# Optimization experiments

Measured on AMD Instinct MI355X. Metric: run time of the kernel, lower is better.

Reference implementation:

```python
import jax, jax.numpy as jnp
import numpy as np

EMBED_DIM = 2048
NUM_HEADS = 32
NUM_KV_HEADS = 8
HEAD_DIM = EMBED_DIM // NUM_HEADS          # 64
GROUP = NUM_HEADS // NUM_KV_HEADS          # 4 queries per KV head
BATCH, SEQ = 2, 2048


def setup_inputs() -> dict:
    key = jax.random.key(0)
    ks = jax.random.split(key, 9)
    s_in = 1.0 / np.sqrt(EMBED_DIM)
    kv_dim = NUM_KV_HEADS * HEAD_DIM
    return {
        "x":      jax.random.normal(ks[0], (BATCH, SEQ, EMBED_DIM), jnp.float32),
        "Wq":     jax.random.normal(ks[1], (EMBED_DIM, EMBED_DIM), jnp.float32) * s_in,
        "bq":     jnp.zeros((EMBED_DIM,), jnp.float32),
        "Wk":     jax.random.normal(ks[2], (EMBED_DIM, kv_dim), jnp.float32) * s_in,
        "bk":     jnp.zeros((kv_dim,), jnp.float32),
        "Wv":     jax.random.normal(ks[3], (EMBED_DIM, kv_dim), jnp.float32) * s_in,
        "bv":     jnp.zeros((kv_dim,), jnp.float32),
        "Wo":     jax.random.normal(ks[4], (EMBED_DIM, EMBED_DIM), jnp.float32) * s_in,
        "bo":     jnp.zeros((EMBED_DIM,), jnp.float32),
    }


def reference(x, Wq, bq, Wk, bk, Wv, bv, Wo, bo):
    B, S, _ = x.shape
    # Projections (torch Linear == x @ W + b with W stored as [in, out] here)
    q = (x @ Wq + bq).reshape(B, S, NUM_KV_HEADS, GROUP, HEAD_DIM)  # grouped heads
    k = (x @ Wk + bk).reshape(B, S, NUM_KV_HEADS, HEAD_DIM)
    v = (x @ Wv + bv).reshape(B, S, NUM_KV_HEADS, HEAD_DIM)

    scale = 1.0 / np.sqrt(HEAD_DIM)
    # scores[b, h, g, s, t] = q[b, s, h, g, :] . k[b, t, h, :]
    # (repeat_interleave of K across the group dim == broadcasting over g)
    scores = jnp.einsum("bshgd,bthd->bhgst", q, k) * scale
    attn = jax.nn.softmax(scores, axis=-1)
    out = jnp.einsum("bhgst,bthd->bshgd", attn, v)  # [B, S, kvh, g, D]
    out = out.reshape(B, S, EMBED_DIM)
    return out @ Wo + bo
```

## Files before the change

### kernel.cpp

```cpp
#include <hip/hip_runtime.h>


typedef __attribute__((ext_vector_type(8)))  short     s16x8;
typedef __attribute__((ext_vector_type(8)))  _Float16  h8;
typedef __attribute__((ext_vector_type(2)))  __fp16    fp16x2;
typedef __attribute__((ext_vector_type(4)))  float     f32x4;
typedef __attribute__((ext_vector_type(16))) float     f32x16;

#define DEVI static __device__ __forceinline__

#if __has_builtin(__builtin_amdgcn_exp2f)
#define EXP2F __builtin_amdgcn_exp2f
#else
#define EXP2F exp2f
#endif

DEVI short f2h(float f){ _Float16 h = (_Float16)f; return __builtin_bit_cast(short, h); }
DEVI unsigned pkh(float a, float b){
  fp16x2 t = __builtin_amdgcn_cvt_pkrtz(a, b);
  return __builtin_bit_cast(unsigned, t);
}

typedef __attribute__((address_space(3))) unsigned       lds_u32;
typedef __attribute__((address_space(1))) const unsigned gbl_u32;
DEVI void glds16(const short* g, short* l){
  __builtin_amdgcn_global_load_lds((gbl_u32*)g, (lds_u32*)l, 16, 0, 0);
}

__global__ void cast_kernel(const float* __restrict__ in, short* __restrict__ out, int n){
  int i = (blockIdx.x * 256 + threadIdx.x) * 8;
  if(i >= n) return;
  float4 a = *(const float4*)(in + i);
  float4 b = *(const float4*)(in + i + 4);
  s16x8 v;
  v[0]=f2h(a.x); v[1]=f2h(a.y); v[2]=f2h(a.z); v[3]=f2h(a.w);
  v[4]=f2h(b.x); v[5]=f2h(b.y); v[6]=f2h(b.z); v[7]=f2h(b.w);
  *(s16x8*)(out + i) = v;
}

__global__ void prep_kernel(const float* __restrict__ Wq, const float* __restrict__ Wk,
                            const float* __restrict__ Wv, const float* __restrict__ Wo,
                            const float* __restrict__ bq, const float* __restrict__ bk,
                            const float* __restrict__ bv,
                            short* __restrict__ WT, short* __restrict__ WoT,
                            float* __restrict__ bqkv){
  __shared__ __align__(16) short tile[64*72];
  const int gy = blockIdx.y;
  const int t = threadIdx.x;
  if(gy >= 80){
    int i = blockIdx.x * 256 + t;
    if(i < 3072) bqkv[i] = (i < 2048) ? bq[i] : (i < 2560 ? bk[i-2048] : bv[i-2560]);
    return;
  }
  const float* src; short* dst; int ldin, by;
  if(gy < 32)      { src = Wq; dst = WT;             ldin = 2048; by = gy;    }
  else if(gy < 40) { src = Wk; dst = WT + 2048*2048; ldin =  512; by = gy-32; }
  else if(gy < 48) { src = Wv; dst = WT + 2560*2048; ldin =  512; by = gy-40; }
  else             { src = Wo; dst = WoT;            ldin = 2048; by = gy-48; }
  const int tr = blockIdx.x * 64;
  const int tc = by * 64;
  for(int c = t; c < 512; c += 256){
    int r = c >> 3, g = c & 7;
    const float* p = src + (size_t)(tr + r) * ldin + tc + g*8;
    s16x8 v;
    #pragma unroll
    for(int e = 0; e < 8; e++) v[e] = f2h(p[e]);
    *(s16x8*)&tile[r*72 + g*8] = v;
  }
  __syncthreads();
  for(int c = t; c < 512; c += 256){
    int r = c >> 3, g = c & 7;
    s16x8 v;
    #pragma unroll
    for(int e = 0; e < 8; e++) v[e] = tile[(g*8+e)*72 + r];
    *(s16x8*)(dst + (size_t)(tc + r) * 2048 + tr + g*8) = v;
  }
}

__global__ void transpose_h_kernel(const short* __restrict__ in, short* __restrict__ out,
                                   int ldin, int ldout){
  __shared__ __align__(16) short tile[64*72];
  const int tr = blockIdx.x * 64;
  const int tc = blockIdx.y * 64;
  const int t = threadIdx.x;
  for(int c = t; c < 512; c += 256){
    int r = c >> 3, g = c & 7;
    *(s16x8*)&tile[r*72 + g*8] = *(const s16x8*)(in + (size_t)(tr + r) * ldin + tc + g*8);
  }
  __syncthreads();
  for(int c = t; c < 512; c += 256){
    int r = c >> 3, g = c & 7;
    s16x8 v;
    #pragma unroll
    for(int e = 0; e < 8; e++) v[e] = tile[(g*8+e)*72 + r];
    *(s16x8*)(out + (size_t)(tc + r) * ldout + tr + g*8) = v;
  }
}

template<bool OUT_F32>
__global__ __launch_bounds__(256, 2)
void gemm_bt_kernel(const short* __restrict__ A, const short* __restrict__ BT,
                    const float* __restrict__ bias, void* __restrict__ C,
                    int M, int N, int K, int scale_cols, float qscale){
  __shared__ __align__(16) short As[128*32];
  __shared__ __align__(16) short Bs[128*32];
  const int m0 = blockIdx.x * 128;
  const int n0 = blockIdx.y * 128;
  const int tid = threadIdx.x;
  const int wave = tid >> 6, lane = tid & 63;
  const int l16 = lane & 15, quad = lane >> 4;
  const int wm = (wave >> 1) * 64, wn = (wave & 1) * 64;

  const short* gA = A  + (size_t)(m0 + wave*32 + (lane>>2))*K + (lane&3)*8;
  const short* gB = BT + (size_t)(n0 + wave*32 + (lane>>2))*K + (lane&3)*8;
  short* lA = As + wave*32*32;
  short* lB = Bs + wave*32*32;

  f32x4 acc[4][4];
  #pragma unroll
  for(int i=0;i<4;i++)
    #pragma unroll
    for(int j=0;j<4;j++) acc[i][j] = (f32x4)(0.0f);

  for(int k0 = 0; k0 < K; k0 += 32){
    glds16(gA + k0,                lA);
    glds16(gA + 16*(size_t)K + k0, lA + 512);
    glds16(gB + k0,                lB);
    glds16(gB + 16*(size_t)K + k0, lB + 512);
    __syncthreads();
    h8 af[4], bfr[4];
    #pragma unroll
    for(int i=0;i<4;i++){
      af[i]  = *(const h8*)&As[(wm + i*16 + l16)*32 + quad*8];
      bfr[i] = *(const h8*)&Bs[(wn + i*16 + l16)*32 + quad*8];
    }
    #pragma unroll
    for(int i=0;i<4;i++)
      #pragma unroll
      for(int j=0;j<4;j++)
        acc[i][j] = __builtin_amdgcn_mfma_f32_16x16x32_f16(af[i], bfr[j], acc[i][j], 0, 0, 0);
    __syncthreads();
  }

  #pragma unroll
  for(int j=0;j<4;j++){
    int col = n0 + wn + j*16 + l16;
    float bb = bias[col];
    float sc = (col < scale_cols) ? qscale : 1.0f;
    #pragma unroll
    for(int i=0;i<4;i++){
      #pragma unroll
      for(int r=0;r<4;r++){
        size_t row = (size_t)(m0 + wm + i*16 + quad*4 + r);
        float v = (acc[i][j][r] + bb) * sc;
        if(OUT_F32) ((float*)C)[row*(size_t)N + col] = v;
        else        ((short*)C)[row*(size_t)N + col] = f2h(v);
      }
    }
  }
}

__global__ __launch_bounds__(256, 2)
void attn_kernel(const short* __restrict__ Qg, const short* __restrict__ Kg,
                 const short* __restrict__ VT, short* __restrict__ Og, int ldq){
  const int qt  = blockIdx.x;
  const int kvh = blockIdx.y;
  const int b   = blockIdx.z;
  const int tid = threadIdx.x;
  const int wave = tid >> 6, lane = tid & 63;
  const int c = lane & 31, h = lane >> 5;
  const int head = kvh*4 + wave;
  const int q0 = qt * 64;

  __shared__ __align__(16) short Ks[2][64*72];
  __shared__ __align__(16) short Vs[2][64*72];

  h8 qreg[4][2];
  #pragma unroll
  for(int ks2=0; ks2<4; ks2++)
    #pragma unroll
    for(int qg=0; qg<2; qg++)
      qreg[ks2][qg] = *(const h8*)(Qg + (size_t)(b*2048 + q0 + qg*32 + c)*ldq
                                      + head*64 + ks2*16 + h*8);

  float lsum[2] = {0.0f, 0.0f};
  f32x16 oacc[2][2];
  #pragma unroll
  for(int qg=0; qg<2; qg++)
    #pragma unroll
    for(int mb=0; mb<2; mb++) oacc[qg][mb] = (f32x16)(0.0f);

  const short* gK = Kg + (size_t)(b*2048 + (tid>>3))*ldq + kvh*64 + (tid&7)*8;
  const short* gV = VT + (size_t)(kvh*64 + (tid>>3))*4096 + b*2048 + (tid&7)*8;
  const int so = (tid>>3)*72 + (tid&7)*8;
  const size_t kHalf = (size_t)32 * ldq;

  s16x8 kr0 = *(const s16x8*)(gK);
  s16x8 kr1 = *(const s16x8*)(gK + kHalf);
  s16x8 vr0 = *(const s16x8*)(gV);
  s16x8 vr1 = *(const s16x8*)(gV + 32*4096);

  for(int t0 = 0; t0 < 2048; t0 += 64){
    const int buf = (t0 >> 6) & 1;
    short* sK = &Ks[buf][so];
    short* sV = &Vs[buf][so];
    *(s16x8*)sK           = kr0;
    *(s16x8*)(sK + 32*72) = kr1;
    *(s16x8*)sV           = vr0;
    *(s16x8*)(sV + 32*72) = vr1;
    __syncthreads();
    if(t0 + 64 < 2048){
      const short* nK = gK + (size_t)(t0 + 64)*ldq;
      const short* nV = gV + (t0 + 64);
      kr0 = *(const s16x8*)(nK);
      kr1 = *(const s16x8*)(nK + kHalf);
      vr0 = *(const s16x8*)(nV);
      vr1 = *(const s16x8*)(nV + 32*4096);
    }
    const short* Kbuf = Ks[buf];
    const short* Vbuf = Vs[buf];

    #pragma unroll
    for(int kb=0; kb<2; kb++){
      f32x16 st[2];
      st[0] = (f32x16)(0.0f); st[1] = (f32x16)(0.0f);
      #pragma unroll
      for(int ks2=0; ks2<4; ks2++){
        h8 ak = *(const h8*)&Kbuf[(kb*32 + c)*72 + ks2*16 + h*8];
        st[0] = __builtin_amdgcn_mfma_f32_32x32x16_f16(ak, qreg[ks2][0], st[0], 0, 0, 0);
        st[1] = __builtin_amdgcn_mfma_f32_32x32x16_f16(ak, qreg[ks2][1], st[1], 0, 0, 0);
      }

      union H8U { h8 v; unsigned u[4]; };
      H8U pk[2][2];
      #pragma unroll
      for(int qg=0; qg<2; qg++){
        float sacc = 0.0f;
        #pragma unroll
        for(int j=0; j<4; j++){
          float pa = EXP2F(st[qg][2*j]);
          float pb = EXP2F(st[qg][2*j+1]);
          sacc += pa + pb;
          pk[qg][0].u[j] = pkh(pa, pb);
        }
        #pragma unroll
        for(int j=0; j<4; j++){
          float pa = EXP2F(st[qg][8+2*j]);
          float pb = EXP2F(st[qg][8+2*j+1]);
          sacc += pa + pb;
          pk[qg][1].u[j] = pkh(pa, pb);
        }
        lsum[qg] += sacc;
      }

      #pragma unroll
      for(int ksp=0; ksp<2; ksp++){
        #pragma unroll
        for(int mb=0; mb<2; mb++){
          const short* vb = &Vbuf[(mb*32 + c)*72 + kb*32 + ksp*16 + h*4];
          H8U av;
          *(uint2*)&av.u[0] = *(const uint2*)(vb);
          *(uint2*)&av.u[2] = *(const uint2*)(vb + 8);
          oacc[0][mb] = __builtin_amdgcn_mfma_f32_32x32x16_f16(av.v, pk[0][ksp].v, oacc[0][mb], 0, 0, 0);
          oacc[1][mb] = __builtin_amdgcn_mfma_f32_32x32x16_f16(av.v, pk[1][ksp].v, oacc[1][mb], 0, 0, 0);
        }
      }
    }
  }

  #pragma unroll
  for(int qg=0; qg<2; qg++){
    lsum[qg] += __shfl_xor(lsum[qg], 32);
    float li = 1.0f / lsum[qg];
    size_t rowoff = (size_t)(b*2048 + q0 + qg*32 + c)*2048 + head*64;
    #pragma unroll
    for(int mb=0; mb<2; mb++){
      #pragma unroll
      for(int g2=0; g2<4; g2++){
        int d0 = mb*32 + 8*g2 + 4*h;
        uint2 w;
        w.x = pkh(oacc[qg][mb][4*g2+0]*li, oacc[qg][mb][4*g2+1]*li);
        w.y = pkh(oacc[qg][mb][4*g2+2]*li, oacc[qg][mb][4*g2+3]*li);
        *(uint2*)&Og[rowoff + d0] = w;
      }
    }
  }
}

extern "C" void kernel_launch(void* const* d_in, const int* in_sizes, int n_in,
                              void* d_out, int out_size, void* d_ws, size_t ws_size,
                              hipStream_t stream){
  const float* x  = (const float*)d_in[0];
  const float* Wq = (const float*)d_in[1];
  const float* bq = (const float*)d_in[2];
  const float* Wk = (const float*)d_in[3];
  const float* bk = (const float*)d_in[4];
  const float* Wv = (const float*)d_in[5];
  const float* bv = (const float*)d_in[6];
  const float* Wo = (const float*)d_in[7];
  const float* bo = (const float*)d_in[8];

  char* ws = (char*)d_ws;
  short* WT   = (short*)(ws);
  short* WoT  = (short*)(ws + 25165824);
  short* xb   = (short*)(ws + 33554432);
  short* QKV  = (short*)(ws + 50331648);
  short* VTb  = (short*)(ws + 75497472);
  float* bqkv = (float*)(ws + 79691776);
  short* AO   = xb;

  cast_kernel<<<4096, 256, 0, stream>>>(x, xb, 8388608);
  prep_kernel<<<dim3(32,81), 256, 0, stream>>>(Wq, Wk, Wv, Wo, bq, bk, bv, WT, WoT, bqkv);

  gemm_bt_kernel<false><<<dim3(32,24), 256, 0, stream>>>(xb, WT, bqkv, QKV,
                                                         4096, 3072, 2048,
                                                         2048, 0.1803368801111244f);

  transpose_h_kernel<<<dim3(64,8), 256, 0, stream>>>(QKV + 2560, VTb, 3072, 4096);

  attn_kernel<<<dim3(32,8,2), 256, 0, stream>>>(QKV, QKV + 2048, VTb, AO, 3072);

  gemm_bt_kernel<true><<<dim3(32,16), 256, 0, stream>>>(AO, WoT, bo, (float*)d_out,
                                                        4096, 2048, 2048, 0, 1.0f);
}
```

Measured before the change: 322.7 us.

## Split attention KV sequence across two wave groups and combine partials in LDS

Doubles the attention block to 512 threads: two groups of four waves each process half of the key/value sequence for the same query tile, then the second group writes its partial output accumulators and row sums to shared memory and the first group adds them before normalizing and storing. This targets low occupancy and per-block latency in the attention kernel, which previously had only 512 blocks of 4 waves. The V tile row stride is also changed to 76 to reduce LDS bank conflicts. Shared memory per block grows, and the combine step adds extra LDS traffic and barriers.

Measured after the change: 1.035 ms. 221% more time.

```diff
diff --git a/kernel.cpp b/kernel.cpp
--- a/kernel.cpp
+++ b/kernel.cpp
@@ -160,7 +160,11 @@
   }
 }
 
-__global__ __launch_bounds__(256, 2)
+#define KS_STRIDE 72
+#define VS_STRIDE 76
+#define GRP_SZ (64*KS_STRIDE + 64*VS_STRIDE)
+
+__global__ __launch_bounds__(512, 4)
 void attn_kernel(const short* __restrict__ Qg, const short* __restrict__ Kg,
                  const short* __restrict__ VT, short* __restrict__ Og, int ldq){
   const int qt  = blockIdx.x;
@@ -168,12 +172,13 @@
   const int b   = blockIdx.z;
   const int tid = threadIdx.x;
   const int wave = tid >> 6, lane = tid & 63;
+  const int gw = wave >> 2;
+  const int w4 = wave & 3;
   const int c = lane & 31, h = lane >> 5;
-  const int head = kvh*4 + wave;
+  const int head = kvh*4 + w4;
   const int q0 = qt * 64;
 
-  __shared__ __align__(16) short Ks[2][64*72];
-  __shared__ __align__(16) short Vs[2][64*72];
+  __shared__ __align__(16) short smem[2*2*GRP_SZ];
 
   h8 qreg[4][2];
   #pragma unroll
@@ -190,9 +195,12 @@
     #pragma unroll
     for(int mb=0; mb<2; mb++) oacc[qg][mb] = (f32x16)(0.0f);
 
-  const short* gK = Kg + (size_t)(b*2048 + (tid>>3))*ldq + kvh*64 + (tid&7)*8;
-  const short* gV = VT + (size_t)(kvh*64 + (tid>>3))*4096 + b*2048 + (tid&7)*8;
-  const int so = (tid>>3)*72 + (tid&7)*8;
+  const int t8 = tid & 255;
+  const int kbase = gw * 1024;
+  const short* gK = Kg + (size_t)(b*2048 + kbase + (t8>>3))*ldq + kvh*64 + (t8&7)*8;
+  const short* gV = VT + (size_t)(kvh*64 + (t8>>3))*4096 + b*2048 + kbase + (t8&7)*8;
+  const int soK = (t8>>3)*KS_STRIDE + (t8&7)*8;
+  const int soV = (t8>>3)*VS_STRIDE + (t8&7)*8;
   const size_t kHalf = (size_t)32 * ldq;
 
   s16x8 kr0 = *(const s16x8*)(gK);
@@ -200,16 +208,15 @@
   s16x8 vr0 = *(const s16x8*)(gV);
   s16x8 vr1 = *(const s16x8*)(gV + 32*4096);
 
-  for(int t0 = 0; t0 < 2048; t0 += 64){
+  for(int t0 = 0; t0 < 1024; t0 += 64){
     const int buf = (t0 >> 6) & 1;
-    short* sK = &Ks[buf][so];
-    short* sV = &Vs[buf][so];
-    *(s16x8*)sK           = kr0;
-    *(s16x8*)(sK + 32*72) = kr1;
-    *(s16x8*)sV           = vr0;
-    *(s16x8*)(sV + 32*72) = vr1;
+    short* base = smem + (gw*2 + buf)*GRP_SZ;
+    *(s16x8*)(base + soK)                     = kr0;
+    *(s16x8*)(base + soK + 32*KS_STRIDE)      = kr1;
+    *(s16x8*)(base + 64*KS_STRIDE + soV)                = vr0;
+    *(s16x8*)(base + 64*KS_STRIDE + soV + 32*VS_STRIDE) = vr1;
     __syncthreads();
-    if(t0 + 64 < 2048){
+    if(t0 + 64 < 1024){
       const short* nK = gK + (size_t)(t0 + 64)*ldq;
       const short* nV = gV + (t0 + 64);
       kr0 = *(const s16x8*)(nK);
@@ -217,8 +224,8 @@
       vr0 = *(const s16x8*)(nV);
       vr1 = *(const s16x8*)(nV + 32*4096);
     }
-    const short* Kbuf = Ks[buf];
-    const short* Vbuf = Vs[buf];
+    const short* Kbuf = smem + (gw*2 + buf)*GRP_SZ;
+    const short* Vbuf = Kbuf + 64*KS_STRIDE;
 
     #pragma unroll
     for(int kb=0; kb<2; kb++){
@@ -226,7 +233,7 @@
       st[0] = (f32x16)(0.0f); st[1] = (f32x16)(0.0f);
       #pragma unroll
       for(int ks2=0; ks2<4; ks2++){
-        h8 ak = *(const h8*)&Kbuf[(kb*32 + c)*72 + ks2*16 + h*8];
+        h8 ak = *(const h8*)&Kbuf[(kb*32 + c)*KS_STRIDE + ks2*16 + h*8];
         st[0] = __builtin_amdgcn_mfma_f32_32x32x16_f16(ak, qreg[ks2][0], st[0], 0, 0, 0);
         st[1] = __builtin_amdgcn_mfma_f32_32x32x16_f16(ak, qreg[ks2][1], st[1], 0, 0, 0);
       }
@@ -257,7 +264,7 @@
       for(int ksp=0; ksp<2; ksp++){
         #pragma unroll
         for(int mb=0; mb<2; mb++){
-          const short* vb = &Vbuf[(mb*32 + c)*72 + kb*32 + ksp*16 + h*4];
+          const short* vb = &Vbuf[(mb*32 + c)*VS_STRIDE + kb*32 + ksp*16 + h*4];
           H8U av;
           *(uint2*)&av.u[0] = *(const uint2*)(vb);
           *(uint2*)&av.u[2] = *(const uint2*)(vb + 8);
@@ -268,6 +275,41 @@
     }
   }
 
+  __syncthreads();
+  float* comb  = (float*)smem;
+  float* lcomb = (float*)smem + 16384;
+  if(gw == 1){
+    #pragma unroll
+    for(int qg=0; qg<2; qg++){
+      lcomb[(w4*2 + qg)*64 + lane] = lsum[qg];
+      #pragma unroll
+      for(int mb=0; mb<2; mb++){
+        #pragma unroll
+        for(int g2=0; g2<4; g2++){
+          f32x4 q4;
+          q4[0] = oacc[qg][mb][4*g2+0]; q4[1] = oacc[qg][mb][4*g2+1];
+          q4[2] = oacc[qg][mb][4*g2+2]; q4[3] = oacc[qg][mb][4*g2+3];
+          *(f32x4*)&comb[(((w4*4 + qg*2 + mb)*4 + g2)*64 + lane)*4] = q4;
+        }
+      }
+    }
+  }
+  __syncthreads();
+  if(gw == 1) return;
+  #pragma unroll
+  for(int qg=0; qg<2; qg++){
+    lsum[qg] += lcomb[(w4*2 + qg)*64 + lane];
+    #pragma unroll
+    for(int mb=0; mb<2; mb++){
+      #pragma unroll
+      for(int g2=0; g2<4; g2++){
+        f32x4 q4 = *(const f32x4*)&comb[(((w4*4 + qg*2 + mb)*4 + g2)*64 + lane)*4];
+        oacc[qg][mb][4*g2+0] += q4[0]; oacc[qg][mb][4*g2+1] += q4[1];
+        oacc[qg][mb][4*g2+2] += q4[2]; oacc[qg][mb][4*g2+3] += q4[3];
+      }
+    }
+  }
+
   #pragma unroll
   for(int qg=0; qg<2; qg++){
     lsum[qg] += __shfl_xor(lsum[qg], 32);
@@ -278,10 +320,10 @@
       #pragma unroll
       for(int g2=0; g2<4; g2++){
         int d0 = mb*32 + 8*g2 + 4*h;
-        uint2 w;
-        w.x = pkh(oacc[qg][mb][4*g2+0]*li, oacc[qg][mb][4*g2+1]*li);
-        w.y = pkh(oacc[qg][mb][4*g2+2]*li, oacc[qg][mb][4*g2+3]*li);
-        *(uint2*)&Og[rowoff + d0] = w;
+        uint2 wv;
+        wv.x = pkh(oacc[qg][mb][4*g2+0]*li, oacc[qg][mb][4*g2+1]*li);
+        wv.y = pkh(oacc[qg][mb][4*g2+2]*li, oacc[qg][mb][4*g2+3]*li);
+        *(uint2*)&Og[rowoff + d0] = wv;
       }
     }
   }
@@ -318,7 +360,7 @@
 
   transpose_h_kernel<<<dim3(64,8), 256, 0, stream>>>(QKV + 2560, VTb, 3072, 4096);
 
-  attn_kernel<<<dim3(32,8,2), 256, 0, stream>>>(QKV, QKV + 2048, VTb, AO, 3072);
+  attn_kernel<<<dim3(32,8,2), 512, 0, stream>>>(QKV, QKV + 2048, VTb, AO, 3072);
 
   gemm_bt_kernel<true><<<dim3(32,16), 256, 0, stream>>>(AO, WoT, bo, (float*)d_out,
                                                         4096, 2048, 2048, 0, 1.0f);
```

## Prepack K/V into MFMA fragment order and stream from global without LDS

Applied to the files above, without the earlier changes.

Replaces the V transpose kernel with a fragpack kernel that writes K and V into per-lane MFMA operand order. The attention kernel then loads its fragments straight from global memory with register double-buffering, which drops LDS staging and the per-tile __syncthreads. It also remaps block IDs so that blocks sharing a KV head are spread across XCDs/CUs. Costs: each wave re-reads K/V from global/L2 rather than sharing it through LDS, and Kf/Vf reuse the WT workspace region, which is only safe if WT is no longer needed.

Measured after the change: 317.2 us. About the same (-1.7%).

```diff
diff --git a/kernel.cpp b/kernel.cpp
--- a/kernel.cpp
+++ b/kernel.cpp
@@ -77,26 +77,6 @@
   }
 }
 
-__global__ void transpose_h_kernel(const short* __restrict__ in, short* __restrict__ out,
-                                   int ldin, int ldout){
-  __shared__ __align__(16) short tile[64*72];
-  const int tr = blockIdx.x * 64;
-  const int tc = blockIdx.y * 64;
-  const int t = threadIdx.x;
-  for(int c = t; c < 512; c += 256){
-    int r = c >> 3, g = c & 7;
-    *(s16x8*)&tile[r*72 + g*8] = *(const s16x8*)(in + (size_t)(tr + r) * ldin + tc + g*8);
-  }
-  __syncthreads();
-  for(int c = t; c < 512; c += 256){
-    int r = c >> 3, g = c & 7;
-    s16x8 v;
-    #pragma unroll
-    for(int e = 0; e < 8; e++) v[e] = tile[(g*8+e)*72 + r];
-    *(s16x8*)(out + (size_t)(tc + r) * ldout + tr + g*8) = v;
-  }
-}
-
 template<bool OUT_F32>
 __global__ __launch_bounds__(256, 2)
 void gemm_bt_kernel(const short* __restrict__ A, const short* __restrict__ BT,
@@ -160,21 +140,54 @@
   }
 }
 
+__global__ void fragpack_kernel(const short* __restrict__ QKV,
+                                short* __restrict__ Kf, short* __restrict__ Vf){
+  __shared__ __align__(16) short kt[64*72];
+  __shared__ __align__(16) short vt[64*72];
+  const int t = blockIdx.x, kvh = blockIdx.y, b = blockIdx.z;
+  const int tid = threadIdx.x;
+  const size_t rowbase = (size_t)(b*2048 + t*64);
+  for(int c = tid; c < 512; c += 256){
+    int r = c >> 3, g = c & 7;
+    const short* src = QKV + (rowbase + r)*3072 + kvh*64 + g*8;
+    *(s16x8*)&kt[r*72 + g*8] = *(const s16x8*)(src + 2048);
+    *(s16x8*)&vt[r*72 + g*8] = *(const s16x8*)(src + 2560);
+  }
+  __syncthreads();
+  const size_t obase = ((size_t)(b*8 + kvh)*32 + t) * 4096;
+  for(int ch = tid; ch < 512; ch += 256){
+    int kb = ch >> 8, l = ch & 63;
+    int c = l & 31, h = l >> 5;
+    int ks2 = (ch >> 6) & 3;
+    *(s16x8*)(Kf + obase + (size_t)ch*8) =
+        *(const s16x8*)&kt[(kb*32 + c)*72 + ks2*16 + h*8];
+    int ksp = (ch >> 7) & 1, mb = (ch >> 6) & 1;
+    int k0 = kb*32 + ksp*16 + h*4;
+    int d  = mb*32 + c;
+    s16x8 v;
+    #pragma unroll
+    for(int j = 0; j < 4; j++){
+      v[j]   = vt[(k0 + j)*72 + d];
+      v[4+j] = vt[(k0 + 8 + j)*72 + d];
+    }
+    *(s16x8*)(Vf + obase + (size_t)ch*8) = v;
+  }
+}
+
 __global__ __launch_bounds__(256, 2)
-void attn_kernel(const short* __restrict__ Qg, const short* __restrict__ Kg,
-                 const short* __restrict__ VT, short* __restrict__ Og, int ldq){
-  const int qt  = blockIdx.x;
-  const int kvh = blockIdx.y;
-  const int b   = blockIdx.z;
+void attn_kernel(const short* __restrict__ Qg, const short* __restrict__ Kf,
+                 const short* __restrict__ Vf, short* __restrict__ Og, int ldq){
+  const int L = blockIdx.x;
+  const int nid = (L & 7)*64 + (L >> 3);
+  const int qt  = nid & 31;
+  const int grp = nid >> 5;
+  const int kvh = grp & 7, b = grp >> 3;
   const int tid = threadIdx.x;
   const int wave = tid >> 6, lane = tid & 63;
   const int c = lane & 31, h = lane >> 5;
   const int head = kvh*4 + wave;
   const int q0 = qt * 64;
 
-  __shared__ __align__(16) short Ks[2][64*72];
-  __shared__ __align__(16) short Vs[2][64*72];
-
   h8 qreg[4][2];
   #pragma unroll
   for(int ks2=0; ks2<4; ks2++)
@@ -190,82 +203,67 @@
     #pragma unroll
     for(int mb=0; mb<2; mb++) oacc[qg][mb] = (f32x16)(0.0f);
 
-  const short* gK = Kg + (size_t)(b*2048 + (tid>>3))*ldq + kvh*64 + (tid&7)*8;
-  const short* gV = VT + (size_t)(kvh*64 + (tid>>3))*4096 + b*2048 + (tid&7)*8;
-  const int so = (tid>>3)*72 + (tid&7)*8;
-  const size_t kHalf = (size_t)32 * ldq;
-
-  s16x8 kr0 = *(const s16x8*)(gK);
-  s16x8 kr1 = *(const s16x8*)(gK + kHalf);
-  s16x8 vr0 = *(const s16x8*)(gV);
-  s16x8 vr1 = *(const s16x8*)(gV + 32*4096);
-
-  for(int t0 = 0; t0 < 2048; t0 += 64){
-    const int buf = (t0 >> 6) & 1;
-    short* sK = &Ks[buf][so];
-    short* sV = &Vs[buf][so];
-    *(s16x8*)sK           = kr0;
-    *(s16x8*)(sK + 32*72) = kr1;
-    *(s16x8*)sV           = vr0;
-    *(s16x8*)(sV + 32*72) = vr1;
-    __syncthreads();
-    if(t0 + 64 < 2048){
-      const short* nK = gK + (size_t)(t0 + 64)*ldq;
-      const short* nV = gV + (t0 + 64);
-      kr0 = *(const s16x8*)(nK);
-      kr1 = *(const s16x8*)(nK + kHalf);
-      vr0 = *(const s16x8*)(nV);
-      vr1 = *(const s16x8*)(nV + 32*4096);
-    }
-    const short* Kbuf = Ks[buf];
-    const short* Vbuf = Vs[buf];
-
-    #pragma unroll
-    for(int kb=0; kb<2; kb++){
-      f32x16 st[2];
-      st[0] = (f32x16)(0.0f); st[1] = (f32x16)(0.0f);
-      #pragma unroll
-      for(int ks2=0; ks2<4; ks2++){
-        h8 ak = *(const h8*)&Kbuf[(kb*32 + c)*72 + ks2*16 + h*8];
-        st[0] = __builtin_amdgcn_mfma_f32_32x32x16_f16(ak, qreg[ks2][0], st[0], 0, 0, 0);
-        st[1] = __builtin_amdgcn_mfma_f32_32x32x16_f16(ak, qreg[ks2][1], st[1], 0, 0, 0);
-      }
-
-      union H8U { h8 v; unsigned u[4]; };
-      H8U pk[2][2];
-      #pragma unroll
-      for(int qg=0; qg<2; qg++){
-        float sacc = 0.0f;
-        #pragma unroll
-        for(int j=0; j<4; j++){
-          float pa = EXP2F(st[qg][2*j]);
-          float pb = EXP2F(st[qg][2*j+1]);
-          sacc += pa + pb;
-          pk[qg][0].u[j] = pkh(pa, pb);
-        }
-        #pragma unroll
-        for(int j=0; j<4; j++){
-          float pa = EXP2F(st[qg][8+2*j]);
-          float pb = EXP2F(st[qg][8+2*j+1]);
-          sacc += pa + pb;
-          pk[qg][1].u[j] = pkh(pa, pb);
-        }
-        lsum[qg] += sacc;
-      }
-
-      #pragma unroll
-      for(int ksp=0; ksp<2; ksp++){
-        #pragma unroll
-        for(int mb=0; mb<2; mb++){
-          const short* vb = &Vbuf[(mb*32 + c)*72 + kb*32 + ksp*16 + h*4];
-          H8U av;
-          *(uint2*)&av.u[0] = *(const uint2*)(vb);
-          *(uint2*)&av.u[2] = *(const uint2*)(vb + 8);
-          oacc[0][mb] = __builtin_amdgcn_mfma_f32_32x32x16_f16(av.v, pk[0][ksp].v, oacc[0][mb], 0, 0, 0);
-          oacc[1][mb] = __builtin_amdgcn_mfma_f32_32x32x16_f16(av.v, pk[1][ksp].v, oacc[1][mb], 0, 0, 0);
-        }
-      }
-    }
+  const short* kp = Kf + (size_t)grp * 131072 + lane*8;
+  const short* vp = Vf + (size_t)grp * 131072 + lane*8;
+
+  h8 kA[4], vA[4], kB[4], vB[4];
+
+  auto loadf = [&](size_t it, h8* K, h8* V){
+    const short* kq = kp + it*2048;
+    const short* vq = vp + it*2048;
+    #pragma unroll
+    for(int i=0;i<4;i++){
+      K[i] = *(const h8*)(kq + i*512);
+      V[i] = *(const h8*)(vq + i*512);
+    }
+  };
+
+  auto compute = [&](const h8* K, const h8* V){
+    f32x16 st[2];
+    st[0] = (f32x16)(0.0f); st[1] = (f32x16)(0.0f);
+    #pragma unroll
+    for(int ks2=0; ks2<4; ks2++){
+      st[0] = __builtin_amdgcn_mfma_f32_32x32x16_f16(K[ks2], qreg[ks2][0], st[0], 0, 0, 0);
+      st[1] = __builtin_amdgcn_mfma_f32_32x32x16_f16(K[ks2], qreg[ks2][1], st[1], 0, 0, 0);
+    }
+    union H8U { h8 v; unsigned u[4]; };
+    H8U pk[2][2];
+    #pragma unroll
+    for(int qg=0; qg<2; qg++){
+      float sacc = 0.0f;
+      #pragma unroll
+      for(int j=0; j<4; j++){
+        float pa = EXP2F(st[qg][2*j]);
+        float pb = EXP2F(st[qg][2*j+1]);
+        sacc += pa + pb;
+        pk[qg][0].u[j] = pkh(pa, pb);
+      }
+      #pragma unroll
+      for(int j=0; j<4; j++){
+        float pa = EXP2F(st[qg][8+2*j]);
+        float pb = EXP2F(st[qg][8+2*j+1]);
+        sacc += pa + pb;
+        pk[qg][1].u[j] = pkh(pa, pb);
+      }
+      lsum[qg] += sacc;
+    }
+    #pragma unroll
+    for(int ksp=0; ksp<2; ksp++){
+      #pragma unroll
+      for(int mb=0; mb<2; mb++){
+        oacc[0][mb] = __builtin_amdgcn_mfma_f32_32x32x16_f16(V[ksp*2+mb], pk[0][ksp].v, oacc[0][mb], 0, 0, 0);
+        oacc[1][mb] = __builtin_amdgcn_mfma_f32_32x32x16_f16(V[ksp*2+mb], pk[1][ksp].v, oacc[1][mb], 0, 0, 0);
+      }
+    }
+  };
+
+  loadf(0, kA, vA);
+  #pragma unroll 1
+  for(int it = 0; it < 64; it += 2){
+    loadf((size_t)(it+1), kB, vB);
+    compute(kA, vA);
+    loadf((size_t)(it+2 < 64 ? it+2 : 0), kA, vA);
+    compute(kB, vB);
   }
 
   #pragma unroll
@@ -278,10 +276,10 @@
       #pragma unroll
       for(int g2=0; g2<4; g2++){
         int d0 = mb*32 + 8*g2 + 4*h;
-        uint2 w;
-        w.x = pkh(oacc[qg][mb][4*g2+0]*li, oacc[qg][mb][4*g2+1]*li);
-        w.y = pkh(oacc[qg][mb][4*g2+2]*li, oacc[qg][mb][4*g2+3]*li);
-        *(uint2*)&Og[rowoff + d0] = w;
+        uint2 wv;
+        wv.x = pkh(oacc[qg][mb][4*g2+0]*li, oacc[qg][mb][4*g2+1]*li);
+        wv.y = pkh(oacc[qg][mb][4*g2+2]*li, oacc[qg][mb][4*g2+3]*li);
+        *(uint2*)&Og[rowoff + d0] = wv;
       }
     }
   }
@@ -305,9 +303,10 @@
   short* WoT  = (short*)(ws + 25165824);
   short* xb   = (short*)(ws + 33554432);
   short* QKV  = (short*)(ws + 50331648);
-  short* VTb  = (short*)(ws + 75497472);
   float* bqkv = (float*)(ws + 79691776);
   short* AO   = xb;
+  short* Kf   = (short*)(ws);
+  short* Vf   = (short*)(ws + 4194304);
 
   cast_kernel<<<4096, 256, 0, stream>>>(x, xb, 8388608);
   prep_kernel<<<dim3(32,81), 256, 0, stream>>>(Wq, Wk, Wv, Wo, bq, bk, bv, WT, WoT, bqkv);
@@ -316,9 +315,9 @@
                                                          4096, 3072, 2048,
                                                          2048, 0.1803368801111244f);
 
-  transpose_h_kernel<<<dim3(64,8), 256, 0, stream>>>(QKV + 2560, VTb, 3072, 4096);
-
-  attn_kernel<<<dim3(32,8,2), 256, 0, stream>>>(QKV, QKV + 2048, VTb, AO, 3072);
+  fragpack_kernel<<<dim3(32,8,2), 256, 0, stream>>>(QKV, Kf, Vf);
+
+  attn_kernel<<<512, 256, 0, stream>>>(QKV, Kf, Vf, AO, 3072);
 
   gemm_bt_kernel<true><<<dim3(32,16), 256, 0, stream>>>(AO, WoT, bo, (float*)d_out,
                                                         4096, 2048, 2048, 0, 1.0f);
```
